# Kernel optimization log

Measured on AMD Instinct MI355X. Metric: run time of the kernel, lower is better.

## Reference

```python
import jax, jax.numpy as jnp
import numpy as np

INPUT_DIM = 512
OUTPUT_DIM = 512
NUM_BASIS = 16
GRID_MIN, GRID_MAX = -2.0, 2.0
LN_EPS = 1e-5


def rbf_basis(x):
    # x: [batch, input_dim] -> [batch, input_dim, num_basis]
    centers = jnp.linspace(GRID_MIN, GRID_MAX, NUM_BASIS, dtype=x.dtype)  # [K]
    h = (GRID_MAX - GRID_MIN) / (NUM_BASIS - 1)
    z = (x[..., None] - centers) / h
    return jnp.exp(-(z * z))


def setup_inputs() -> dict:
    key = jax.random.key(0)
    k1, k2, k3 = jax.random.split(key, 3)
    x = jax.random.normal(k1, (4096, INPUT_DIM), dtype=jnp.float32)
    weights = jax.random.normal(k2, (OUTPUT_DIM, INPUT_DIM, NUM_BASIS), dtype=jnp.float32) * 0.1
    base_weights = jax.random.normal(k3, (OUTPUT_DIM, INPUT_DIM), dtype=jnp.float32) * 0.1
    ln_gamma = jnp.ones((OUTPUT_DIM,), dtype=jnp.float32)
    ln_beta = jnp.zeros((OUTPUT_DIM,), dtype=jnp.float32)
    return {"x": x, "weights": weights, "base_weights": base_weights,
            "ln_gamma": ln_gamma, "ln_beta": ln_beta}


def reference(x, weights, base_weights, ln_gamma, ln_beta):
    # per-edge basis expansion: [B, I, K]
    basis = rbf_basis(x)
    # fused contraction replacing the nested python loops:
    # out[b, j] = sum_{i,k} basis[b, i, k] * weights[j, i, k]
    out = jnp.einsum('bik,jik->bj', basis, weights)
    # residual base activation path
    out = out + jax.nn.silu(x) @ base_weights.T
    # layer norm over output_dim
    mean = jnp.mean(out, axis=-1, keepdims=True)
    var = jnp.var(out, axis=-1, keepdims=True)
    out = (out - mean) * jax.lax.rsqrt(var + LN_EPS) * ln_gamma + ln_beta
    return out
```

## Files before the change

kernel.cpp:

```cpp
#include <hip/hip_runtime.h>
#include <hip/hip_bf16.h>


typedef __bf16 bf16x8 __attribute__((ext_vector_type(8)));
typedef __bf16 bf16x4 __attribute__((ext_vector_type(4)));
typedef float  f32x4  __attribute__((ext_vector_type(4)));

#define KT 8704
#define SPLITS 8
#define KS (KT / SPLITS)
#define NIT (KS / 32)
#define CPE (4096 * 512)
#define LBUF (128 * 32)

__device__ __forceinline__ void gll16(const __bf16* g, __bf16* l) {
    __builtin_amdgcn_global_load_lds(
        (const __attribute__((address_space(1))) void*)g,
        (__attribute__((address_space(3))) void*)l, 16, 0, 0);
}

__global__ void prep_AB(const float* __restrict__ x, const float* __restrict__ W,
                        const float* __restrict__ Wb, __bf16* __restrict__ A,
                        __bf16* __restrict__ B) {
    if (blockIdx.x < 8192) {
        int t = blockIdx.x * 256 + threadIdx.x;
        int b = t >> 9;
        int i = t & 511;
        float xv = x[t];
        float zb = 3.75f * xv + 7.5f;
        bf16x8 lo, hi;
#pragma unroll
        for (int k = 0; k < 8; ++k) { float z = zb - (float)k; lo[k]   = (__bf16)__expf(-z * z); }
#pragma unroll
        for (int k = 8; k < 16; ++k){ float z = zb - (float)k; hi[k-8] = (__bf16)__expf(-z * z); }
        size_t base = (size_t)b * KT + (size_t)i * 16;
        *(bf16x8*)(A + base)     = lo;
        *(bf16x8*)(A + base + 8) = hi;
        float s = xv / (1.0f + __expf(-xv));
        A[(size_t)b * KT + 8192 + i] = (__bf16)s;
    } else {
        int t = (blockIdx.x - 8192) * 256 + threadIdx.x;
        int j = t / 2176;
        int c = (t - j * 2176) * 4;
        float4 v;
        if (c < 8192) v = *(const float4*)&W[(size_t)j * 8192 + c];
        else          v = *(const float4*)&Wb[(size_t)j * 512 + (c - 8192)];
        bf16x4 o;
        o[0] = (__bf16)v.x; o[1] = (__bf16)v.y; o[2] = (__bf16)v.z; o[3] = (__bf16)v.w;
        *(bf16x4*)&B[(size_t)j * KT + c] = o;
    }
}

__global__ __launch_bounds__(256, 4) void gemm_bt(const __bf16* __restrict__ A,
                                                  const __bf16* __restrict__ B,
                                                  __bf16* __restrict__ Cp) {
    __shared__ __attribute__((aligned(16))) __bf16 As[2 * LBUF];
    __shared__ __attribute__((aligned(16))) __bf16 Bs[2 * LBUF];

    const int tid  = threadIdx.x;
    const int wave = tid >> 6, lane = tid & 63;
    const int q    = lane >> 4, r16 = lane & 15;
    const int m0 = blockIdx.x * 128, n0 = blockIdx.y * 128, k0 = blockIdx.z * KS;
    const int wm = wave & 1, wn = wave >> 1;

    const int row0 = tid >> 2, qk0 = (tid & 3) ^ ((row0 >> 1) & 3);
    const int row1 = row0 + 64, qk1 = (tid & 3) ^ ((row1 >> 1) & 3);
    const __bf16* gA0 = A + (size_t)(m0 + row0) * KT + k0 + qk0 * 8;
    const __bf16* gA1 = A + (size_t)(m0 + row1) * KT + k0 + qk1 * 8;
    const __bf16* gB0 = B + (size_t)(n0 + row0) * KT + k0 + qk0 * 8;
    const __bf16* gB1 = B + (size_t)(n0 + row1) * KT + k0 + qk1 * 8;

    f32x4 acc[4][4] = {};

    const int qa = q ^ ((r16 >> 1) & 3);
    const int awOff = (wm * 64 + r16) * 32 + qa * 8;
    const int bwOff = (wn * 64 + r16) * 32 + qa * 8;

    gll16(gA0, &As[tid * 8]);
    gll16(gA1, &As[(tid + 256) * 8]);
    gll16(gB0, &Bs[tid * 8]);
    gll16(gB1, &Bs[(tid + 256) * 8]);
    __syncthreads();

    for (int it = 0; it < NIT; ++it) {
        const int ko = (it + 1) * 32;
        const int sb = ((it + 1) & 1) * LBUF;
        gll16(gA0 + ko, &As[sb + tid * 8]);
        gll16(gA1 + ko, &As[sb + (tid + 256) * 8]);
        gll16(gB0 + ko, &Bs[sb + tid * 8]);
        gll16(gB1 + ko, &Bs[sb + (tid + 256) * 8]);

        const int cb = (it & 1) * LBUF;
        const __bf16* Aw = &As[cb + awOff];
        const __bf16* Bw = &Bs[cb + bwOff];
        bf16x8 af[4], bg[4];
#pragma unroll
        for (int mi = 0; mi < 4; ++mi) af[mi] = *(const bf16x8*)(Aw + mi * 512);
#pragma unroll
        for (int ni = 0; ni < 4; ++ni) bg[ni] = *(const bf16x8*)(Bw + ni * 512);
#pragma unroll
        for (int mi = 0; mi < 4; ++mi)
#pragma unroll
            for (int ni = 0; ni < 4; ++ni)
                acc[mi][ni] = __builtin_amdgcn_mfma_f32_16x16x32_bf16(
                    af[mi], bg[ni], acc[mi][ni], 0, 0, 0);

        __syncthreads();
    }

    __bf16* Cb = Cp + (size_t)blockIdx.z * CPE;
#pragma unroll
    for (int mi = 0; mi < 4; ++mi) {
        const int row = m0 + wm * 64 + mi * 16 + q * 4;
#pragma unroll
        for (int ni = 0; ni < 4; ++ni) {
            const int col = n0 + wn * 64 + ni * 16 + r16;
#pragma unroll
            for (int r = 0; r < 4; ++r)
                Cb[(size_t)(row + r) * 512 + col] = (__bf16)acc[mi][ni][r];
        }
    }
}

__global__ void ln_kernel(const __bf16* __restrict__ Cp, const float* __restrict__ gamma,
                          const float* __restrict__ beta, float* __restrict__ out) {
    const int tid  = threadIdx.x;
    const int wave = tid >> 6, lane = tid & 63;
    const int row  = blockIdx.x * 4 + wave;
    const size_t base = (size_t)row * 512 + lane * 8;

    float v[8] = {};
    float s = 0.f, s2 = 0.f;
#pragma unroll
    for (int z = 0; z < SPLITS; ++z) {
        bf16x8 p = *(const bf16x8*)(Cp + (size_t)z * CPE + base);
#pragma unroll
        for (int j = 0; j < 8; ++j) v[j] += (float)p[j];
    }
#pragma unroll
    for (int j = 0; j < 8; ++j) { s += v[j]; s2 += v[j] * v[j]; }
#pragma unroll
    for (int m = 32; m >= 1; m >>= 1) {
        s  += __shfl_xor(s, m);
        s2 += __shfl_xor(s2, m);
    }
    const float mean = s * (1.0f / 512.0f);
    const float var  = s2 * (1.0f / 512.0f) - mean * mean;
    const float rs   = rsqrtf(var + 1e-5f);
    float4 o0, o1;
    const float4 g0 = *(const float4*)&gamma[lane * 8];
    const float4 g1 = *(const float4*)&gamma[lane * 8 + 4];
    const float4 b0 = *(const float4*)&beta[lane * 8];
    const float4 b1 = *(const float4*)&beta[lane * 8 + 4];
    o0.x = (v[0] - mean) * rs * g0.x + b0.x;
    o0.y = (v[1] - mean) * rs * g0.y + b0.y;
    o0.z = (v[2] - mean) * rs * g0.z + b0.z;
    o0.w = (v[3] - mean) * rs * g0.w + b0.w;
    o1.x = (v[4] - mean) * rs * g1.x + b1.x;
    o1.y = (v[5] - mean) * rs * g1.y + b1.y;
    o1.z = (v[6] - mean) * rs * g1.z + b1.z;
    o1.w = (v[7] - mean) * rs * g1.w + b1.w;
    *(float4*)&out[base]     = o0;
    *(float4*)&out[base + 4] = o1;
}

extern "C" void kernel_launch(void* const* d_in, const int* in_sizes, int n_in,
                              void* d_out, int out_size, void* d_ws, size_t ws_size,
                              hipStream_t stream) {
    const float* x     = (const float*)d_in[0];
    const float* W     = (const float*)d_in[1];
    const float* Wb    = (const float*)d_in[2];
    const float* gamma = (const float*)d_in[3];
    const float* beta  = (const float*)d_in[4];
    float* out = (float*)d_out;

    char* ws = (char*)d_ws;
    __bf16* A  = (__bf16*)ws;
    __bf16* Bm = (__bf16*)(ws + 71303168);
    __bf16* Cp = (__bf16*)(ws + 80216064);

    prep_AB<<<8192 + 4352, 256, 0, stream>>>(x, W, Wb, A, Bm);
    dim3 g(32, 4, SPLITS);
    gemm_bt<<<g, 256, 0, stream>>>(A, Bm, Cp);
    ln_kernel<<<1024, 256, 0, stream>>>(Cp, gamma, beta, out);
}
```

Measured before the change: 150.6 us.

## Triple-buffer LDS in split-K GEMM with vmcnt waits and MFMA priority

Turns the double-buffered global_load_lds pipeline in the bf16 GEMM into a three-stage ring, so tiles are prefetched two iterations ahead. The full __syncthreads is replaced by an explicit s_waitcnt vmcnt(4) plus s_barrier, so only the older tile's loads must finish before each barrier. The MFMA block is also wrapped in s_setprio to favour math issue. The cost is 48KB of LDS per block, so occupancy drops from 4 to 3 blocks per CU, which the launch bounds now reflect.

```diff
diff --git a/kernel.cpp b/kernel.cpp
--- a/kernel.cpp
+++ b/kernel.cpp
@@ -51,11 +51,11 @@
     }
 }
 
-__global__ __launch_bounds__(256, 4) void gemm_bt(const __bf16* __restrict__ A,
+__global__ __launch_bounds__(256, 3) void gemm_bt(const __bf16* __restrict__ A,
                                                   const __bf16* __restrict__ B,
                                                   __bf16* __restrict__ Cp) {
-    __shared__ __attribute__((aligned(16))) __bf16 As[2 * LBUF];
-    __shared__ __attribute__((aligned(16))) __bf16 Bs[2 * LBUF];
+    __shared__ __attribute__((aligned(16))) __bf16 As[3 * LBUF];
+    __shared__ __attribute__((aligned(16))) __bf16 Bs[3 * LBUF];
 
     const int tid  = threadIdx.x;
     const int wave = tid >> 6, lane = tid & 63;
@@ -76,37 +76,48 @@
     const int awOff = (wm * 64 + r16) * 32 + qa * 8;
     const int bwOff = (wn * 64 + r16) * 32 + qa * 8;
 
-    gll16(gA0, &As[tid * 8]);
-    gll16(gA1, &As[(tid + 256) * 8]);
-    gll16(gB0, &Bs[tid * 8]);
-    gll16(gB1, &Bs[(tid + 256) * 8]);
-    __syncthreads();
+    auto stage = [&](int t, int sb) {
+        const int ko = t * 32;
+        const int so = sb * LBUF;
+        gll16(gA0 + ko, &As[so + tid * 8]);
+        gll16(gA1 + ko, &As[so + (tid + 256) * 8]);
+        gll16(gB0 + ko, &Bs[so + tid * 8]);
+        gll16(gB1 + ko, &Bs[so + (tid + 256) * 8]);
+    };
 
-    for (int it = 0; it < NIT; ++it) {
-        const int ko = (it + 1) * 32;
-        const int sb = ((it + 1) & 1) * LBUF;
-        gll16(gA0 + ko, &As[sb + tid * 8]);
-        gll16(gA1 + ko, &As[sb + (tid + 256) * 8]);
-        gll16(gB0 + ko, &Bs[sb + tid * 8]);
-        gll16(gB1 + ko, &Bs[sb + (tid + 256) * 8]);
-
-        const int cb = (it & 1) * LBUF;
-        const __bf16* Aw = &As[cb + awOff];
-        const __bf16* Bw = &Bs[cb + bwOff];
+    auto compute = [&](int cb) {
+        const __bf16* Aw = &As[cb * LBUF + awOff];
+        const __bf16* Bw = &Bs[cb * LBUF + bwOff];
         bf16x8 af[4], bg[4];
 #pragma unroll
         for (int mi = 0; mi < 4; ++mi) af[mi] = *(const bf16x8*)(Aw + mi * 512);
 #pragma unroll
         for (int ni = 0; ni < 4; ++ni) bg[ni] = *(const bf16x8*)(Bw + ni * 512);
+        __builtin_amdgcn_s_setprio(1);
 #pragma unroll
         for (int mi = 0; mi < 4; ++mi)
 #pragma unroll
             for (int ni = 0; ni < 4; ++ni)
                 acc[mi][ni] = __builtin_amdgcn_mfma_f32_16x16x32_bf16(
                     af[mi], bg[ni], acc[mi][ni], 0, 0, 0);
+        __builtin_amdgcn_s_setprio(0);
+    };
 
-        __syncthreads();
+    stage(0, 0);
+    stage(1, 1);
+    asm volatile("s_waitcnt vmcnt(4)" ::: "memory");
+    __builtin_amdgcn_s_barrier();
+
+    int cb = 0;
+    for (int it = 0; it < NIT - 1; ++it) {
+        int sb = cb - 1; if (sb < 0) sb = 2;
+        stage(it + 2, sb);
+        compute(cb);
+        asm volatile("s_waitcnt vmcnt(4)" ::: "memory");
+        __builtin_amdgcn_s_barrier();
+        cb = (cb == 2) ? 0 : cb + 1;
     }
+    compute(cb);
 
     __bf16* Cb = Cp + (size_t)blockIdx.z * CPE;
 #pragma unroll
```

New measurement: 152.2 us. Within noise of the previous version (+1.1%).
